# Optimization experiments

Measured on AMD Instinct MI355X. Metric: run time of the kernel, lower is better.

Reference implementation:

```python
import jax, jax.numpy as jnp
import numpy as np

B, N = 64, 4096          # batch of diagrams, points per diagram
H, W = 64, 64            # persistence-image resolution
L, R = 5, 256            # num_landscapes, landscape resolution
EPS = 1e-8


def setup_inputs() -> dict:
    key = jax.random.key(0)
    k1, = jax.random.split(key, 1)
    u = jax.random.uniform(k1, (B, N, 2), dtype=jnp.float32)
    birth = u[..., 0] * 0.5                      # births in [0, 0.5]
    death = birth + u[..., 1] * 0.5 + 1e-3       # deaths > births, in range
    pairs = jnp.stack([birth, death], axis=-1)   # (B, N, 2)
    sigma = jnp.float32(0.1)                     # learned bandwidth (nn.Parameter)
    return {"pairs": pairs, "sigma": sigma}


def reference(pairs, sigma):
    # ---- Persistence image (batched, vectorized over points) ----
    grid_x = jnp.linspace(0.0, 1.0, W, dtype=pairs.dtype)   # birth axis
    grid_y = jnp.linspace(0.0, 1.0, H, dtype=pairs.dtype)   # persistence axis
    birth = pairs[..., 0]                 # (B, N)
    death = pairs[..., 1]                 # (B, N)
    pers = death - birth                  # (B, N)
    # normalization per config ranges (0,1): divide by (range + 1e-8)
    birth_n = birth / (1.0 + EPS)
    pers_n = pers / (1.0 + EPS)
    weights = pers                        # weight_fn == 'linear'
    inv2s2 = 1.0 / (2.0 * sigma * sigma)
    # separable Gaussian factors: (B, N, W) and (B, N, H)
    gx = jnp.exp(-(grid_x[None, None, :] - birth_n[..., None]) ** 2 * inv2s2)
    gy = jnp.exp(-(grid_y[None, None, :] - pers_n[..., None]) ** 2 * inv2s2)
    # sum_n wt_n * gy_n(h) * gx_n(w)  ->  (B, H, W)
    image = jnp.einsum('bnh,bnw->bhw', gy * weights[..., None], gx)
    image = image / (jnp.max(image, axis=(1, 2), keepdims=True) + EPS)

    # ---- Persistence landscapes ----
    min_b = jnp.min(birth, axis=1, keepdims=True)   # (B, 1)
    max_d = jnp.max(death, axis=1, keepdims=True)   # (B, 1)
    frac = jnp.linspace(0.0, 1.0, R, dtype=pairs.dtype)
    t = min_b + (max_d - min_b) * frac[None, :]     # (B, R)
    rising = jnp.clip(t[:, None, :] - birth[..., None], 0.0)   # (B, N, R)
    falling = jnp.clip(death[..., None] - t[:, None, :], 0.0)  # (B, N, R)
    tents = jnp.minimum(rising, falling)                        # (B, N, R)
    # descending sort over points + take top L == top_k over point axis
    top = jax.lax.top_k(jnp.swapaxes(tents, 1, 2), L)[0]        # (B, R, L)
    landscapes = jnp.swapaxes(top, 1, 2)                        # (B, L, R)
    return image, landscapes
```

## Files before the change

### kernel.cpp

```cpp
#include <hip/hip_runtime.h>
#include <math.h>


#define B_   64
#define N_   4096
#define HW_  64
#define RES_ 256
#define EPSF 1e-8f
#define KC_  4
#define CPB  1024
#define KP   64

typedef short short8v  __attribute__((ext_vector_type(8)));
typedef float float4v  __attribute__((ext_vector_type(4)));

__device__ __forceinline__ unsigned short f2bf(float f) {
    unsigned int u = __float_as_uint(f);
    u += 0x7fffu + ((u >> 16) & 1u);
    return (unsigned short)(u >> 16);
}

__global__ __launch_bounds__(256) void k_minmax(const float* __restrict__ pairs,
                                                float* __restrict__ wsf) {
    int b = blockIdx.x, tid = threadIdx.x;
    const float2* pr = (const float2*)pairs + (size_t)b * N_;
    float mn = 1e30f, mx = -1e30f;
    #pragma unroll
    for (int i = 0; i < N_ / 256; ++i) {
        float2 v = pr[tid + i * 256];
        mn = fminf(mn, v.x);
        mx = fmaxf(mx, v.y);
    }
    #pragma unroll
    for (int off = 32; off > 0; off >>= 1) {
        mn = fminf(mn, __shfl_xor(mn, off, 64));
        mx = fmaxf(mx, __shfl_xor(mx, off, 64));
    }
    __shared__ float smn[4], smx[4];
    if ((tid & 63) == 0) { smn[tid >> 6] = mn; smx[tid >> 6] = mx; }
    __syncthreads();
    if (tid == 0) {
        mn = fminf(fminf(smn[0], smn[1]), fminf(smn[2], smn[3]));
        mx = fmaxf(fmaxf(smx[0], smx[1]), fmaxf(smx[2], smx[3]));
        wsf[b]      = mn;
        wsf[64 + b] = mx;
    }
}

__global__ __launch_bounds__(256) void k_img_stage(const float* __restrict__ pairs,
                                                   const float* __restrict__ sigp,
                                                   float* __restrict__ part) {
    __shared__ unsigned short gy_lds[64 * 72];
    __shared__ unsigned short gx_lds[64 * 72];
    __shared__ float2 pts_lds[CPB];

    int kc = blockIdx.x, b = blockIdx.y;
    int tid = threadIdx.x;
    int l = tid & 63, w = tid >> 6;

    float sigma = sigp[0];
    float cc = 0.5f / (sigma * sigma);

    const float4* src = (const float4*)(pairs + 2 * ((size_t)b * N_ + kc * CPB));
    ((float4*)pts_lds)[tid]       = src[tid];
    ((float4*)pts_lds)[256 + tid] = src[256 + tid];

    int c  = tid & 63;
    int pg = tid >> 6;
    float xc = (float)c * (1.0f / 63.0f);

    float4v acc[4];
    #pragma unroll
    for (int c4 = 0; c4 < 4; ++c4) acc[c4] = (float4v){0.f, 0.f, 0.f, 0.f};

    int rowA = (w * 16 + (l & 15)) * 72 + (l >> 4) * 8;

    for (int ch = 0; ch < CPB / KP; ++ch) {
        __syncthreads();
        int p0 = ch * KP + pg * 16;
        alignas(16) unsigned short gyb[16], gxb[16];
        #pragma unroll
        for (int j = 0; j < 16; ++j) {
            float2 q = pts_lds[p0 + j];
            float pe = q.y - q.x;
            float dx = xc - q.x;
            float dy = xc - pe;
            gxb[j] = f2bf(__expf(-dx * dx * cc));
            gyb[j] = f2bf(pe * __expf(-dy * dy * cc));
        }
        *(uint4*)&gy_lds[c * 72 + pg * 16]     = *(uint4*)&gyb[0];
        *(uint4*)&gy_lds[c * 72 + pg * 16 + 8] = *(uint4*)&gyb[8];
        *(uint4*)&gx_lds[c * 72 + pg * 16]     = *(uint4*)&gxb[0];
        *(uint4*)&gx_lds[c * 72 + pg * 16 + 8] = *(uint4*)&gxb[8];
        __syncthreads();
        #pragma unroll
        for (int ks = 0; ks < 2; ++ks) {
            short8v af = *(const short8v*)&gy_lds[rowA + ks * 32];
            #pragma unroll
            for (int c4 = 0; c4 < 4; ++c4) {
                short8v bf = *(const short8v*)
                    &gx_lds[(c4 * 16 + (l & 15)) * 72 + ks * 32 + (l >> 4) * 8];
                acc[c4] = __builtin_amdgcn_mfma_f32_16x16x32_bf16(af, bf, acc[c4], 0, 0, 0);
            }
        }
    }

    float* dst = part + (size_t)(b * KC_ + kc) * (HW_ * HW_);
    #pragma unroll
    for (int c4 = 0; c4 < 4; ++c4)
        #pragma unroll
        for (int reg = 0; reg < 4; ++reg) {
            int h = w * 16 + (l >> 4) * 4 + reg;
            int wv = c4 * 16 + (l & 15);
            dst[h * HW_ + wv] = acc[c4][reg];
        }
}

__global__ __launch_bounds__(256) void k_img_reduce(const float* __restrict__ part,
                                                    float* __restrict__ img,
                                                    float* __restrict__ bmax) {
    int blk = blockIdx.x, b = blockIdx.y, tid = threadIdx.x;
    int pix4 = blk * 256 + tid;
    const float4* p0 = (const float4*)(part + (size_t)b * KC_ * (HW_ * HW_));
    float4 s = p0[pix4];
    #pragma unroll
    for (int kc = 1; kc < KC_; ++kc) {
        float4 v = p0[(size_t)kc * 1024 + pix4];
        s.x += v.x; s.y += v.y; s.z += v.z; s.w += v.w;
    }
    ((float4*)(img + (size_t)b * (HW_ * HW_)))[pix4] = s;
    float m = fmaxf(fmaxf(s.x, s.y), fmaxf(s.z, s.w));
    #pragma unroll
    for (int off = 32; off > 0; off >>= 1) m = fmaxf(m, __shfl_xor(m, off, 64));
    __shared__ float sm[4];
    if ((tid & 63) == 0) sm[tid >> 6] = m;
    __syncthreads();
    if (tid == 0)
        bmax[b * 4 + blk] = fmaxf(fmaxf(sm[0], sm[1]), fmaxf(sm[2], sm[3]));
}

__global__ __launch_bounds__(256) void k_img_scale(const float* __restrict__ img,
                                                   const float* __restrict__ bmax,
                                                   float* __restrict__ out) {
    int blk = blockIdx.x, b = blockIdx.y, tid = threadIdx.x;
    float m = fmaxf(fmaxf(bmax[b * 4], bmax[b * 4 + 1]),
                    fmaxf(bmax[b * 4 + 2], bmax[b * 4 + 3]));
    float inv = 1.0f / (m + EPSF);
    int pix4 = blk * 256 + tid;
    float4 v = ((const float4*)(img + (size_t)b * (HW_ * HW_)))[pix4];
    v.x *= inv; v.y *= inv; v.z *= inv; v.w *= inv;
    ((float4*)(out + (size_t)b * (HW_ * HW_)))[pix4] = v;
}

__global__ __launch_bounds__(256) void k_land_partial(const float* __restrict__ pairs,
                                                      const float* __restrict__ wsf,
                                                      float* __restrict__ lp, int PC) {
    extern __shared__ float4 pts[];
    int pc = blockIdx.x, b = blockIdx.y, tid = threadIdx.x;
    int chunk = N_ / PC;
    int n0 = pc * chunk;
    int np4 = chunk >> 1;
    const float4* src = (const float4*)(pairs + 2 * ((size_t)b * N_ + n0));
    for (int i = tid; i < np4; i += 256) pts[i] = src[i];
    __syncthreads();

    float minb = wsf[b], maxd = wsf[64 + b];
    float t_r = minb + (maxd - minb) * ((float)tid * (1.0f / 255.0f));

    float v0 = 0.f, v1 = 0.f, v2 = 0.f, v3 = 0.f, v4 = 0.f;
    #pragma unroll 4
    for (int p = 0; p < np4; ++p) {
        float4 q = pts[p];
        {
            float x = fmaxf(fminf(t_r - q.x, q.y - t_r), 0.0f);
            float a;
            a = fmaxf(v0, x); x = fminf(v0, x); v0 = a;
            a = fmaxf(v1, x); x = fminf(v1, x); v1 = a;
            a = fmaxf(v2, x); x = fminf(v2, x); v2 = a;
            a = fmaxf(v3, x); x = fminf(v3, x); v3 = a;
            v4 = fmaxf(v4, x);
        }
        {
            float x = fmaxf(fminf(t_r - q.z, q.w - t_r), 0.0f);
            float a;
            a = fmaxf(v0, x); x = fminf(v0, x); v0 = a;
            a = fmaxf(v1, x); x = fminf(v1, x); v1 = a;
            a = fmaxf(v2, x); x = fminf(v2, x); v2 = a;
            a = fmaxf(v3, x); x = fminf(v3, x); v3 = a;
            v4 = fmaxf(v4, x);
        }
    }
    float* d = lp + ((size_t)(b * PC + pc) * RES_ + tid) * 5;
    d[0] = v0; d[1] = v1; d[2] = v2; d[3] = v3; d[4] = v4;
}

__global__ __launch_bounds__(256) void k_land_merge(const float* __restrict__ lp,
                                                    float* __restrict__ out, int PC) {
    int b = blockIdx.x, r = threadIdx.x;
    const float* s0 = lp + ((size_t)b * PC * RES_ + r) * 5;
    float v0 = s0[0], v1 = s0[1], v2 = s0[2], v3 = s0[3], v4 = s0[4];
    for (int pc = 1; pc < PC; ++pc) {
        const float* sp = lp + ((size_t)(b * PC + pc) * RES_ + r) * 5;
        #pragma unroll
        for (int l = 0; l < 5; ++l) {
            float x = sp[l];
            float a;
            a = fmaxf(v0, x); x = fminf(v0, x); v0 = a;
            a = fmaxf(v1, x); x = fminf(v1, x); v1 = a;
            a = fmaxf(v2, x); x = fminf(v2, x); v2 = a;
            a = fmaxf(v3, x); x = fminf(v3, x); v3 = a;
            v4 = fmaxf(v4, x);
        }
    }
    float* o = out + (size_t)B_ * HW_ * HW_ + (size_t)b * (5 * RES_);
    o[r]            = v0;
    o[RES_ + r]     = v1;
    o[2 * RES_ + r] = v2;
    o[3 * RES_ + r] = v3;
    o[4 * RES_ + r] = v4;
}

extern "C" void kernel_launch(void* const* d_in, const int* in_sizes, int n_in,
                              void* d_out, int out_size, void* d_ws, size_t ws_size,
                              hipStream_t stream) {
    const float* pairs = (const float*)d_in[0];
    const float* sig   = (const float*)d_in[1];
    float* out = (float*)d_out;
    float* wsf = (float*)d_ws;

    size_t availF = ws_size / 4;
    int PC = 16;
    while (PC > 1 &&
           (384 + (size_t)B_ * HW_ * HW_ + (size_t)B_ * PC * RES_ * 5 +
            (size_t)B_ * KC_ * HW_ * HW_) > availF)
        PC >>= 1;
    size_t landF = (size_t)B_ * PC * RES_ * 5;

    float* bmax = wsf + 128;
    float* img  = wsf + 384;
    float* lp   = img + (size_t)B_ * HW_ * HW_;
    float* part = lp + landF;

    k_minmax<<<B_, 256, 0, stream>>>(pairs, wsf);
    k_img_stage<<<dim3(KC_, B_), 256, 0, stream>>>(pairs, sig, part);
    int chunk = N_ / PC;
    k_land_partial<<<dim3(PC, B_), 256, (size_t)chunk * 8, stream>>>(pairs, wsf, lp, PC);
    k_img_reduce<<<dim3(4, B_), 256, 0, stream>>>(part, img, bmax);
    k_img_scale<<<dim3(4, B_), 256, 0, stream>>>(img, bmax, out);
    k_land_merge<<<B_, 256, 0, stream>>>(lp, out, PC);
}
```

Measured before the change: 113.1 us.

## Fuse image and landscape stages into one launch and use med3 top-5 insertion

Merges the image MFMA stage and the landscape partial top-k into a single heterogeneous grid, with 256 image blocks and 512 landscape blocks, so both run concurrently. It also fuses the reduce, scale and landscape merge into one finish kernel, cutting six launches to three. The landscape top-5 insertion now uses fmed3, and each wave handles 4 resolution points over a 128-point chunk read directly from global memory, with no LDS staging. The cost is more partial lists to merge (32 per batch) and dropping the workspace-size fallback, which assumes the workspace is large enough.

```diff
diff --git a/kernel.cpp b/kernel.cpp
--- a/kernel.cpp
+++ b/kernel.cpp
@@ -10,6 +10,8 @@
 #define KC_  4
 #define CPB  1024
 #define KP   64
+#define PCW  32
+#define LCH  (N_ / PCW)
 
 typedef short short8v  __attribute__((ext_vector_type(8)));
 typedef float float4v  __attribute__((ext_vector_type(4)));
@@ -19,6 +21,16 @@
     u += 0x7fffu + ((u >> 16) & 1u);
     return (unsigned short)(u >> 16);
 }
+
+#define INS5(v0, v1, v2, v3, v4, x)                       \
+    {                                                     \
+        float _p0 = v0, _p1 = v1, _p2 = v2, _p3 = v3;     \
+        v0 = fmaxf(_p0, x);                               \
+        v1 = __builtin_amdgcn_fmed3f(_p0, _p1, x);        \
+        v2 = __builtin_amdgcn_fmed3f(_p1, _p2, x);        \
+        v3 = __builtin_amdgcn_fmed3f(_p2, _p3, x);        \
+        v4 = __builtin_amdgcn_fmed3f(_p3, v4, x);         \
+    }
 
 __global__ __launch_bounds__(256) void k_minmax(const float* __restrict__ pairs,
                                                 float* __restrict__ wsf) {
@@ -47,177 +59,180 @@
     }
 }
 
-__global__ __launch_bounds__(256) void k_img_stage(const float* __restrict__ pairs,
-                                                   const float* __restrict__ sigp,
-                                                   float* __restrict__ part) {
+__global__ __launch_bounds__(256) void k_main(const float* __restrict__ pairs,
+                                              const float* __restrict__ sigp,
+                                              const float* __restrict__ wsf,
+                                              float* __restrict__ part,
+                                              float* __restrict__ lp) {
     __shared__ unsigned short gy_lds[64 * 72];
     __shared__ unsigned short gx_lds[64 * 72];
     __shared__ float2 pts_lds[CPB];
 
-    int kc = blockIdx.x, b = blockIdx.y;
     int tid = threadIdx.x;
     int l = tid & 63, w = tid >> 6;
 
-    float sigma = sigp[0];
-    float cc = 0.5f / (sigma * sigma);
-
-    const float4* src = (const float4*)(pairs + 2 * ((size_t)b * N_ + kc * CPB));
-    ((float4*)pts_lds)[tid]       = src[tid];
-    ((float4*)pts_lds)[256 + tid] = src[256 + tid];
-
-    int c  = tid & 63;
-    int pg = tid >> 6;
-    float xc = (float)c * (1.0f / 63.0f);
-
-    float4v acc[4];
-    #pragma unroll
-    for (int c4 = 0; c4 < 4; ++c4) acc[c4] = (float4v){0.f, 0.f, 0.f, 0.f};
-
-    int rowA = (w * 16 + (l & 15)) * 72 + (l >> 4) * 8;
-
-    for (int ch = 0; ch < CPB / KP; ++ch) {
-        __syncthreads();
-        int p0 = ch * KP + pg * 16;
-        alignas(16) unsigned short gyb[16], gxb[16];
-        #pragma unroll
-        for (int j = 0; j < 16; ++j) {
-            float2 q = pts_lds[p0 + j];
-            float pe = q.y - q.x;
-            float dx = xc - q.x;
-            float dy = xc - pe;
-            gxb[j] = f2bf(__expf(-dx * dx * cc));
-            gyb[j] = f2bf(pe * __expf(-dy * dy * cc));
-        }
-        *(uint4*)&gy_lds[c * 72 + pg * 16]     = *(uint4*)&gyb[0];
-        *(uint4*)&gy_lds[c * 72 + pg * 16 + 8] = *(uint4*)&gyb[8];
-        *(uint4*)&gx_lds[c * 72 + pg * 16]     = *(uint4*)&gxb[0];
-        *(uint4*)&gx_lds[c * 72 + pg * 16 + 8] = *(uint4*)&gxb[8];
-        __syncthreads();
-        #pragma unroll
-        for (int ks = 0; ks < 2; ++ks) {
-            short8v af = *(const short8v*)&gy_lds[rowA + ks * 32];
+    if (blockIdx.x < 256) {
+        int kc = blockIdx.x & 3, b = blockIdx.x >> 2;
+        float sigma = sigp[0];
+        float cc = 0.5f / (sigma * sigma);
+
+        const float4* src = (const float4*)(pairs + 2 * ((size_t)b * N_ + kc * CPB));
+        ((float4*)pts_lds)[tid]       = src[tid];
+        ((float4*)pts_lds)[256 + tid] = src[256 + tid];
+
+        int c  = tid & 63;
+        int pg = tid >> 6;
+        float xc = (float)c * (1.0f / 63.0f);
+
+        float4v acc[4];
+        #pragma unroll
+        for (int c4 = 0; c4 < 4; ++c4) acc[c4] = (float4v){0.f, 0.f, 0.f, 0.f};
+
+        int rowA = (w * 16 + (l & 15)) * 72 + (l >> 4) * 8;
+
+        for (int ch = 0; ch < CPB / KP; ++ch) {
+            __syncthreads();
+            int p0 = ch * KP + pg * 16;
+            alignas(16) unsigned short gyb[16], gxb[16];
             #pragma unroll
-            for (int c4 = 0; c4 < 4; ++c4) {
-                short8v bf = *(const short8v*)
-                    &gx_lds[(c4 * 16 + (l & 15)) * 72 + ks * 32 + (l >> 4) * 8];
-                acc[c4] = __builtin_amdgcn_mfma_f32_16x16x32_bf16(af, bf, acc[c4], 0, 0, 0);
-            }
-        }
-    }
-
-    float* dst = part + (size_t)(b * KC_ + kc) * (HW_ * HW_);
-    #pragma unroll
-    for (int c4 = 0; c4 < 4; ++c4)
-        #pragma unroll
-        for (int reg = 0; reg < 4; ++reg) {
-            int h = w * 16 + (l >> 4) * 4 + reg;
-            int wv = c4 * 16 + (l & 15);
-            dst[h * HW_ + wv] = acc[c4][reg];
-        }
-}
-
-__global__ __launch_bounds__(256) void k_img_reduce(const float* __restrict__ part,
-                                                    float* __restrict__ img,
-                                                    float* __restrict__ bmax) {
-    int blk = blockIdx.x, b = blockIdx.y, tid = threadIdx.x;
-    int pix4 = blk * 256 + tid;
+            for (int j = 0; j < 16; ++j) {
+                float2 q = pts_lds[p0 + j];
+                float pe = q.y - q.x;
+                float dx = xc - q.x;
+                float dy = xc - pe;
+                gxb[j] = f2bf(__expf(-dx * dx * cc));
+                gyb[j] = f2bf(pe * __expf(-dy * dy * cc));
+            }
+            *(uint4*)&gy_lds[c * 72 + pg * 16]     = *(uint4*)&gyb[0];
+            *(uint4*)&gy_lds[c * 72 + pg * 16 + 8] = *(uint4*)&gyb[8];
+            *(uint4*)&gx_lds[c * 72 + pg * 16]     = *(uint4*)&gxb[0];
+            *(uint4*)&gx_lds[c * 72 + pg * 16 + 8] = *(uint4*)&gxb[8];
+            __syncthreads();
+            #pragma unroll
+            for (int ks = 0; ks < 2; ++ks) {
+                short8v af = *(const short8v*)&gy_lds[rowA + ks * 32];
+                #pragma unroll
+                for (int c4 = 0; c4 < 4; ++c4) {
+                    short8v bf = *(const short8v*)
+                        &gx_lds[(c4 * 16 + (l & 15)) * 72 + ks * 32 + (l >> 4) * 8];
+                    acc[c4] = __builtin_amdgcn_mfma_f32_16x16x32_bf16(af, bf, acc[c4], 0, 0, 0);
+                }
+            }
+        }
+
+        float* dst = part + (size_t)(b * KC_ + kc) * (HW_ * HW_);
+        #pragma unroll
+        for (int c4 = 0; c4 < 4; ++c4)
+            #pragma unroll
+            for (int reg = 0; reg < 4; ++reg) {
+                int h = w * 16 + (l >> 4) * 4 + reg;
+                int wv = c4 * 16 + (l & 15);
+                dst[h * HW_ + wv] = acc[c4][reg];
+            }
+    } else {
+        int idx = blockIdx.x - 256;
+        int b = idx >> 3, pcb = idx & 7;
+        int pc = pcb * 4 + w;
+        float minb = wsf[b], maxd = wsf[64 + b];
+        float sc = (maxd - minb) * (1.0f / 255.0f);
+        float t0 = minb + sc * (float)l;
+        float t1 = t0 + sc * 64.0f;
+        float t2 = t0 + sc * 128.0f;
+        float t3 = t0 + sc * 192.0f;
+
+        float a0 = 0.f, a1 = 0.f, a2 = 0.f, a3 = 0.f, a4 = 0.f;
+        float b0 = 0.f, b1 = 0.f, b2 = 0.f, b3 = 0.f, b4 = 0.f;
+        float c0 = 0.f, c1 = 0.f, c2 = 0.f, c3 = 0.f, c4 = 0.f;
+        float d0 = 0.f, d1 = 0.f, d2 = 0.f, d3 = 0.f, d4 = 0.f;
+
+        const float4* pw = (const float4*)(pairs + 2 * ((size_t)b * N_ + pc * LCH));
+        #pragma unroll 4
+        for (int p = 0; p < LCH / 2; ++p) {
+            float4 q = pw[p];
+            {
+                float bb = q.x, dd = q.y;
+                float x;
+                x = fminf(t0 - bb, dd - t0); INS5(a0, a1, a2, a3, a4, x);
+                x = fminf(t1 - bb, dd - t1); INS5(b0, b1, b2, b3, b4, x);
+                x = fminf(t2 - bb, dd - t2); INS5(c0, c1, c2, c3, c4, x);
+                x = fminf(t3 - bb, dd - t3); INS5(d0, d1, d2, d3, d4, x);
+            }
+            {
+                float bb = q.z, dd = q.w;
+                float x;
+                x = fminf(t0 - bb, dd - t0); INS5(a0, a1, a2, a3, a4, x);
+                x = fminf(t1 - bb, dd - t1); INS5(b0, b1, b2, b3, b4, x);
+                x = fminf(t2 - bb, dd - t2); INS5(c0, c1, c2, c3, c4, x);
+                x = fminf(t3 - bb, dd - t3); INS5(d0, d1, d2, d3, d4, x);
+            }
+        }
+
+        float* dst = lp + (size_t)(b * PCW + pc) * 5 * RES_;
+        dst[0*RES_ + l]       = a0; dst[1*RES_ + l]       = a1;
+        dst[2*RES_ + l]       = a2; dst[3*RES_ + l]       = a3;
+        dst[4*RES_ + l]       = a4;
+        dst[0*RES_ + l + 64]  = b0; dst[1*RES_ + l + 64]  = b1;
+        dst[2*RES_ + l + 64]  = b2; dst[3*RES_ + l + 64]  = b3;
+        dst[4*RES_ + l + 64]  = b4;
+        dst[0*RES_ + l + 128] = c0; dst[1*RES_ + l + 128] = c1;
+        dst[2*RES_ + l + 128] = c2; dst[3*RES_ + l + 128] = c3;
+        dst[4*RES_ + l + 128] = c4;
+        dst[0*RES_ + l + 192] = d0; dst[1*RES_ + l + 192] = d1;
+        dst[2*RES_ + l + 192] = d2; dst[3*RES_ + l + 192] = d3;
+        dst[4*RES_ + l + 192] = d4;
+    }
+}
+
+__global__ __launch_bounds__(256) void k_finish(const float* __restrict__ part,
+                                                const float* __restrict__ lp,
+                                                float* __restrict__ out) {
+    int b = blockIdx.x, tid = threadIdx.x;
+
     const float4* p0 = (const float4*)(part + (size_t)b * KC_ * (HW_ * HW_));
-    float4 s = p0[pix4];
-    #pragma unroll
-    for (int kc = 1; kc < KC_; ++kc) {
-        float4 v = p0[(size_t)kc * 1024 + pix4];
-        s.x += v.x; s.y += v.y; s.z += v.z; s.w += v.w;
-    }
-    ((float4*)(img + (size_t)b * (HW_ * HW_)))[pix4] = s;
-    float m = fmaxf(fmaxf(s.x, s.y), fmaxf(s.z, s.w));
+    float4 s[4];
+    float m = 0.0f;
+    #pragma unroll
+    for (int i = 0; i < 4; ++i) {
+        int pix4 = tid + i * 256;
+        float4 v = p0[pix4];
+        #pragma unroll
+        for (int kc = 1; kc < KC_; ++kc) {
+            float4 u = p0[(size_t)kc * 1024 + pix4];
+            v.x += u.x; v.y += u.y; v.z += u.z; v.w += u.w;
+        }
+        s[i] = v;
+        m = fmaxf(m, fmaxf(fmaxf(v.x, v.y), fmaxf(v.z, v.w)));
+    }
     #pragma unroll
     for (int off = 32; off > 0; off >>= 1) m = fmaxf(m, __shfl_xor(m, off, 64));
     __shared__ float sm[4];
     if ((tid & 63) == 0) sm[tid >> 6] = m;
     __syncthreads();
-    if (tid == 0)
-        bmax[b * 4 + blk] = fmaxf(fmaxf(sm[0], sm[1]), fmaxf(sm[2], sm[3]));
-}
-
-__global__ __launch_bounds__(256) void k_img_scale(const float* __restrict__ img,
-                                                   const float* __restrict__ bmax,
-                                                   float* __restrict__ out) {
-    int blk = blockIdx.x, b = blockIdx.y, tid = threadIdx.x;
-    float m = fmaxf(fmaxf(bmax[b * 4], bmax[b * 4 + 1]),
-                    fmaxf(bmax[b * 4 + 2], bmax[b * 4 + 3]));
+    m = fmaxf(fmaxf(sm[0], sm[1]), fmaxf(sm[2], sm[3]));
     float inv = 1.0f / (m + EPSF);
-    int pix4 = blk * 256 + tid;
-    float4 v = ((const float4*)(img + (size_t)b * (HW_ * HW_)))[pix4];
-    v.x *= inv; v.y *= inv; v.z *= inv; v.w *= inv;
-    ((float4*)(out + (size_t)b * (HW_ * HW_)))[pix4] = v;
-}
-
-__global__ __launch_bounds__(256) void k_land_partial(const float* __restrict__ pairs,
-                                                      const float* __restrict__ wsf,
-                                                      float* __restrict__ lp, int PC) {
-    extern __shared__ float4 pts[];
-    int pc = blockIdx.x, b = blockIdx.y, tid = threadIdx.x;
-    int chunk = N_ / PC;
-    int n0 = pc * chunk;
-    int np4 = chunk >> 1;
-    const float4* src = (const float4*)(pairs + 2 * ((size_t)b * N_ + n0));
-    for (int i = tid; i < np4; i += 256) pts[i] = src[i];
-    __syncthreads();
-
-    float minb = wsf[b], maxd = wsf[64 + b];
-    float t_r = minb + (maxd - minb) * ((float)tid * (1.0f / 255.0f));
+    float4* od = (float4*)(out + (size_t)b * (HW_ * HW_));
+    #pragma unroll
+    for (int i = 0; i < 4; ++i) {
+        float4 v = s[i];
+        v.x *= inv; v.y *= inv; v.z *= inv; v.w *= inv;
+        od[tid + i * 256] = v;
+    }
 
     float v0 = 0.f, v1 = 0.f, v2 = 0.f, v3 = 0.f, v4 = 0.f;
-    #pragma unroll 4
-    for (int p = 0; p < np4; ++p) {
-        float4 q = pts[p];
-        {
-            float x = fmaxf(fminf(t_r - q.x, q.y - t_r), 0.0f);
-            float a;
-            a = fmaxf(v0, x); x = fminf(v0, x); v0 = a;
-            a = fmaxf(v1, x); x = fminf(v1, x); v1 = a;
-            a = fmaxf(v2, x); x = fminf(v2, x); v2 = a;
-            a = fmaxf(v3, x); x = fminf(v3, x); v3 = a;
-            v4 = fmaxf(v4, x);
-        }
-        {
-            float x = fmaxf(fminf(t_r - q.z, q.w - t_r), 0.0f);
-            float a;
-            a = fmaxf(v0, x); x = fminf(v0, x); v0 = a;
-            a = fmaxf(v1, x); x = fminf(v1, x); v1 = a;
-            a = fmaxf(v2, x); x = fminf(v2, x); v2 = a;
-            a = fmaxf(v3, x); x = fminf(v3, x); v3 = a;
-            v4 = fmaxf(v4, x);
-        }
-    }
-    float* d = lp + ((size_t)(b * PC + pc) * RES_ + tid) * 5;
-    d[0] = v0; d[1] = v1; d[2] = v2; d[3] = v3; d[4] = v4;
-}
-
-__global__ __launch_bounds__(256) void k_land_merge(const float* __restrict__ lp,
-                                                    float* __restrict__ out, int PC) {
-    int b = blockIdx.x, r = threadIdx.x;
-    const float* s0 = lp + ((size_t)b * PC * RES_ + r) * 5;
-    float v0 = s0[0], v1 = s0[1], v2 = s0[2], v3 = s0[3], v4 = s0[4];
-    for (int pc = 1; pc < PC; ++pc) {
-        const float* sp = lp + ((size_t)(b * PC + pc) * RES_ + r) * 5;
-        #pragma unroll
-        for (int l = 0; l < 5; ++l) {
-            float x = sp[l];
-            float a;
-            a = fmaxf(v0, x); x = fminf(v0, x); v0 = a;
-            a = fmaxf(v1, x); x = fminf(v1, x); v1 = a;
-            a = fmaxf(v2, x); x = fminf(v2, x); v2 = a;
-            a = fmaxf(v3, x); x = fminf(v3, x); v3 = a;
-            v4 = fmaxf(v4, x);
+    const float* lpb = lp + (size_t)b * PCW * 5 * RES_;
+    for (int pc = 0; pc < PCW; ++pc) {
+        #pragma unroll
+        for (int lvl = 0; lvl < 5; ++lvl) {
+            float x = lpb[(pc * 5 + lvl) * RES_ + tid];
+            INS5(v0, v1, v2, v3, v4, x);
         }
     }
     float* o = out + (size_t)B_ * HW_ * HW_ + (size_t)b * (5 * RES_);
-    o[r]            = v0;
-    o[RES_ + r]     = v1;
-    o[2 * RES_ + r] = v2;
-    o[3 * RES_ + r] = v3;
-    o[4 * RES_ + r] = v4;
+    o[tid]            = v0;
+    o[RES_ + tid]     = v1;
+    o[2 * RES_ + tid] = v2;
+    o[3 * RES_ + tid] = v3;
+    o[4 * RES_ + tid] = v4;
 }
 
 extern "C" void kernel_launch(void* const* d_in, const int* in_sizes, int n_in,
@@ -228,24 +243,10 @@
     float* out = (float*)d_out;
     float* wsf = (float*)d_ws;
 
-    size_t availF = ws_size / 4;
-    int PC = 16;
-    while (PC > 1 &&
-           (384 + (size_t)B_ * HW_ * HW_ + (size_t)B_ * PC * RES_ * 5 +
-            (size_t)B_ * KC_ * HW_ * HW_) > availF)
-        PC >>= 1;
-    size_t landF = (size_t)B_ * PC * RES_ * 5;
-
-    float* bmax = wsf + 128;
-    float* img  = wsf + 384;
-    float* lp   = img + (size_t)B_ * HW_ * HW_;
-    float* part = lp + landF;
+    float* part = wsf + 128;
+    float* lp   = part + (size_t)B_ * KC_ * HW_ * HW_;
 
     k_minmax<<<B_, 256, 0, stream>>>(pairs, wsf);
-    k_img_stage<<<dim3(KC_, B_), 256, 0, stream>>>(pairs, sig, part);
-    int chunk = N_ / PC;
-    k_land_partial<<<dim3(PC, B_), 256, (size_t)chunk * 8, stream>>>(pairs, wsf, lp, PC);
-    k_img_reduce<<<dim3(4, B_), 256, 0, stream>>>(part, img, bmax);
-    k_img_scale<<<dim3(4, B_), 256, 0, stream>>>(img, bmax, out);
-    k_land_merge<<<B_, 256, 0, stream>>>(lp, out, PC);
-}
+    k_main<<<768, 256, 0, stream>>>(pairs, sig, wsf, part, lp);
+    k_finish<<<B_, 256, 0, stream>>>(part, lp, out);
+}
```

After: 93.85 us. 17.0% less time.
